# Kernel tuning notes

Measured on AMD Instinct MI355X. Metric: run time of the kernel, lower is better.

## Reference

```python
import jax, jax.numpy as jnp
import numpy as np

ITERS = 3
LAMB = 0.05
EPS = 1e-6


def _l2norm(x):
    return x / jnp.clip(jnp.linalg.norm(x, axis=-1, keepdims=True), 1e-8)


def setup_inputs() -> dict:
    key = jax.random.key(0)
    k1, k2, k3, k4 = jax.random.split(key, 4)
    bi, bt, R, W, D = 128, 128, 36, 50, 256
    imgs = jax.random.normal(k1, (bi, R, D), dtype=jnp.float32)
    caps = jax.random.normal(k2, (bt, W, D), dtype=jnp.float32)
    # valid lengths in [1, max]; pin element 0 to max so int(lens.max()) == static dim
    img_lens = jax.random.randint(k3, (bi,), 1, R + 1).at[0].set(R)
    cap_lens = jax.random.randint(k4, (bt,), 1, W + 1).at[0].set(W)
    return {"imgs": imgs, "caps": caps, "img_lens": img_lens, "cap_lens": cap_lens}


def _forward(imgs, caps, img_lens, cap_lens):
    bi, R, D = imgs.shape
    bt, W, _ = caps.shape
    # fine-grained cosine similarities: [bi, bt, R, W]
    fg_sims = jnp.einsum("ird,jwd->ijrw", _l2norm(imgs), _l2norm(caps))
    # mask[i,j,r,w] = (r < img_lens[i]) & (w < cap_lens[j])
    rmask = jnp.arange(R) < img_lens[:, None]          # [bi, R]
    wmask = jnp.arange(W) < cap_lens[:, None]          # [bt, W]
    mask = rmask[:, None, :, None] & wmask[None, :, None, :]  # [bi, bt, R, W]
    maskf = mask.astype(fg_sims.dtype)

    # _ave_init: uniform marginals over valid rows / cols
    r = (mask.sum(axis=-1) != 0).astype(fg_sims.dtype)  # [bi, bt, R]
    r = r / r.sum(axis=-1, keepdims=True)
    c = (mask.sum(axis=-2) != 0).astype(fg_sims.dtype)  # [bi, bt, W]
    c = c / c.sum(axis=-1, keepdims=True)

    # Sinkhorn-Knopp on cost (1 - sims); masked entries get cost=INF -> P=0
    P = jnp.where(mask, jnp.exp(-(1.0 - fg_sims) / LAMB), 0.0)
    P = P / (P.sum(axis=(-2, -1), keepdims=True) + EPS)

    def body(P, _):
        u = P.sum(axis=-1) + EPS          # [bi, bt, R]
        P = P * (r / u)[..., :, None]
        v = P.sum(axis=-2) + EPS          # [bi, bt, W]
        P = P * (c / v)[..., None, :]
        return P, None

    P, _ = jax.lax.scan(body, P, None, length=ITERS)
    sims = (fg_sims * P * maskf).sum(axis=(-2, -1))     # [bi, bt]
    return sims


def reference(imgs, caps, img_lens, cap_lens):
    return _forward(imgs, caps, img_lens, cap_lens)
```

## Files before the change

kernel.cpp:

```cpp
#include <hip/hip_runtime.h>
#include <math.h>

#define BI 128
#define BT 128
#define RR 36
#define WW 50
#define DD 256
#define EPSF 1e-6f
#define EXP2_C1 28.85390081777927f
#define EXP2_C0 (-28.85390081777927f)

#define A_TILES 3
#define B_TILES 4
#define KSTEPS 8
#define A_SLOTS (BI * A_TILES * KSTEPS * 64)
#define B_SLOTS (BT * B_TILES * KSTEPS * 64)

#define CV_AT (BI * A_TILES)
#define CV_BT (BT * B_TILES)

typedef short     v8ss __attribute__((ext_vector_type(8)));
typedef _Float16  v8hf __attribute__((ext_vector_type(8)));
typedef float     v4f  __attribute__((ext_vector_type(4)));

template <typename V>
__device__ __forceinline__ auto mfma_impl(V a, V b, v4f c, int)
    -> decltype(__builtin_amdgcn_mfma_f32_16x16x32_f16(a, b, c, 0, 0, 0)) {
    return __builtin_amdgcn_mfma_f32_16x16x32_f16(a, b, c, 0, 0, 0);
}
template <typename V>
__device__ __forceinline__ v4f mfma_impl(V a, V b, v4f c, long) {
    v8ss a2 = __builtin_bit_cast(v8ss, a);
    v8ss b2 = __builtin_bit_cast(v8ss, b);
    return __builtin_amdgcn_mfma_f32_16x16x32_f16(a2, b2, c, 0, 0, 0);
}
__device__ __forceinline__ v4f mfma_f16(v8hf a, v8hf b, v4f c) {
    return mfma_impl(a, b, c, 0);
}

__device__ __forceinline__ float fast_rcp(float x) {
    return __builtin_amdgcn_rcpf(x);
}
__device__ __forceinline__ float fast_exp2(float x) {
    return __builtin_amdgcn_exp2f(x);
}

template <int N>
__device__ __forceinline__ float dpp_ror_add(float x) {
    int xi = __builtin_bit_cast(int, x);
    int yi = __builtin_amdgcn_update_dpp(xi, xi, 0x120 | N, 0xF, 0xF, false);
    return x + __builtin_bit_cast(float, yi);
}
__device__ __forceinline__ float dpp_sum16(float x) {
    x = dpp_ror_add<1>(x);
    x = dpp_ror_add<2>(x);
    x = dpp_ror_add<4>(x);
    x = dpp_ror_add<8>(x);
    return x;
}

__global__ __launch_bounds__(256) void convert_kernel(
    const float* __restrict__ imgs, const float* __restrict__ caps,
    v8ss* __restrict__ Ah_g, v8ss* __restrict__ Bh_g)
{
    __shared__ float raw[16][260];
    __shared__ float invn[16];

    const int t = threadIdx.x;
    const int b = blockIdx.x;
    const bool isA = b < CV_AT;
    int grp, tile, nrows;
    const float* src;
    if (isA) {
        grp = b / A_TILES; tile = b - grp * A_TILES;
        src = imgs + (size_t)grp * RR * DD;
        nrows = RR;
    } else {
        int bb = b - CV_AT;
        grp = bb / B_TILES; tile = bb - grp * B_TILES;
        src = caps + (size_t)grp * WW * DD;
        nrows = WW;
    }
    const size_t tbase = isA ? (size_t)b * (KSTEPS * 64)
                             : (size_t)(b - CV_AT) * (KSTEPS * 64);
    const int r0 = tile << 4;

    for (int f = t; f < 1024; f += 256) {
        const int row = f >> 6, c4 = f & 63;
        float4 v = make_float4(0.f, 0.f, 0.f, 0.f);
        const int r = r0 + row;
        if (r < nrows) v = *(const float4*)(src + (size_t)r * DD + c4 * 4);
        *(float4*)&raw[row][c4 * 4] = v;
    }
    __syncthreads();

    {
        const int row = t >> 4, seg = t & 15;
        float ss = 0.f;
#pragma unroll
        for (int k = 0; k < 16; ++k) {
            float x = raw[row][k * 16 + seg];
            ss += x * x;
        }
        ss = dpp_sum16(ss);
        if (seg == 0) invn[row] = 1.0f / fmaxf(sqrtf(ss), 1e-8f);
    }
    __syncthreads();

    for (int u = t; u < KSTEPS * 64; u += 256) {
        const int ks = u >> 6, sl = u & 63;
        const int rr = sl & 15, kq = sl >> 4;
        const float inv = invn[rr];
        const float* p = &raw[rr][ks * 32 + kq * 8];
        float4 f0 = *(const float4*)p;
        float4 f1 = *(const float4*)(p + 4);
        float xs[8] = {f0.x, f0.y, f0.z, f0.w, f1.x, f1.y, f1.z, f1.w};
        v8hf h;
#pragma unroll
        for (int e = 0; e < 8; ++e) h[e] = (_Float16)(xs[e] * inv);
        if (isA) Ah_g[tbase + (size_t)ks * 64 + sl] = __builtin_bit_cast(v8ss, h);
        else     Bh_g[tbase + (size_t)ks * 64 + sl] = __builtin_bit_cast(v8ss, h);
    }
}

__global__ __launch_bounds__(64, 4) void pair_kernel(
    const v8ss* __restrict__ Ah_g, const v8ss* __restrict__ Bh_g,
    const int* __restrict__ img_lens, const int* __restrict__ cap_lens,
    float* __restrict__ out)
{
    const int lane = threadIdx.x;
    const int x    = blockIdx.x & 7;
    const int g    = blockIdx.x >> 3;
    const int i    = g >> 4;
    const int j    = (x << 4) + (g & 15);

    const int nr = img_lens[i];
    const int nc = cap_lens[j];
    const int Ma = (nr + 15) >> 4;
    const int Na = (nc + 15) >> 4;

    const v8ss* Ah_b = Ah_g + (size_t)i * (A_TILES * KSTEPS * 64) + lane;
    const v8ss* Bh_b = Bh_g + (size_t)j * (B_TILES * KSTEPS * 64) + lane;

    v4f acc[3][4];
#pragma unroll
    for (int m = 0; m < 3; ++m)
#pragma unroll
        for (int n = 0; n < 4; ++n) acc[m][n] = (v4f){0.f, 0.f, 0.f, 0.f};

    v8hf ah[2][3], bh[2][4];
    auto load_stage = [&](int ks, int buf) {
#pragma unroll
        for (int m = 0; m < 3; ++m) if (m < Ma)
            ah[buf][m] = __builtin_bit_cast(v8hf, Ah_b[(m * KSTEPS + ks) * 64]);
#pragma unroll
        for (int n = 0; n < 4; ++n) if (n < Na)
            bh[buf][n] = __builtin_bit_cast(v8hf, Bh_b[(n * KSTEPS + ks) * 64]);
    };

    load_stage(0, 0);
#pragma unroll
    for (int ks = 0; ks < KSTEPS; ++ks) {
        const int cur = ks & 1;
        if (ks + 1 < KSTEPS) load_stage(ks + 1, cur ^ 1);
#pragma unroll
        for (int n = 0; n < 4; ++n) if (n < Na)
#pragma unroll
            for (int m = 0; m < 3; ++m) if (m < Ma)
                acc[m][n] = mfma_f16(ah[cur][m], bh[cur][n], acc[m][n]);
    }

    const int cl = lane & 15;
    const int rq = (lane >> 4) << 2;
    const float inv_nr = 1.0f / (float)nr;
    const float inv_nc = 1.0f / (float)nc;

    float P0[3][4][4];
    float tot = 0.f;
#pragma unroll
    for (int m = 0; m < 3; ++m) if (m < Ma)
#pragma unroll
        for (int n = 0; n < 4; ++n) if (n < Na)
#pragma unroll
            for (int q = 0; q < 4; ++q) {
                const int row = (m << 4) + rq + q;
                const int col = (n << 4) + cl;
                float pv = 0.f;
                if (row < nr && col < nc)
                    pv = fast_exp2(fmaf(acc[m][n][q], EXP2_C1, EXP2_C0));
                P0[m][n][q] = pv;
                tot += pv;
            }
    tot = dpp_sum16(tot);
    tot += __shfl_xor(tot, 16, 64);
    tot += __shfl_xor(tot, 32, 64);
    const float gsc = fast_rcp(tot + EPSF);

    float u[3][4], v[4];
#pragma unroll
    for (int m = 0; m < 3; ++m)
#pragma unroll
        for (int q = 0; q < 4; ++q) u[m][q] = gsc;
#pragma unroll
    for (int n = 0; n < 4; ++n) v[n] = 1.0f;

#pragma unroll
    for (int it = 0; it < 3; ++it) {
#pragma unroll
        for (int m = 0; m < 3; ++m) if (m < Ma)
#pragma unroll
            for (int q = 0; q < 4; ++q) {
                float d = 0.f;
#pragma unroll
                for (int n = 0; n < 4; ++n) if (n < Na)
                    d = fmaf(P0[m][n][q], v[n], d);
                d = dpp_sum16(d);
                const float t = fmaf(u[m][q], d, EPSF);
                u[m][q] *= inv_nr * fast_rcp(t);
            }
#pragma unroll
        for (int n = 0; n < 4; ++n) if (n < Na) {
            float e = 0.f;
#pragma unroll
            for (int m = 0; m < 3; ++m) if (m < Ma)
#pragma unroll
                for (int q = 0; q < 4; ++q)
                    e = fmaf(P0[m][n][q], u[m][q], e);
            e += __shfl_xor(e, 16, 64);
            e += __shfl_xor(e, 32, 64);
            const float t = fmaf(v[n], e, EPSF);
            v[n] *= inv_nc * fast_rcp(t);
        }
    }

    float osum = 0.f;
#pragma unroll
    for (int m = 0; m < 3; ++m) if (m < Ma)
#pragma unroll
        for (int n = 0; n < 4; ++n) if (n < Na)
#pragma unroll
            for (int q = 0; q < 4; ++q)
                osum = fmaf(acc[m][n][q], P0[m][n][q] * u[m][q] * v[n], osum);
    osum = dpp_sum16(osum);
    osum += __shfl_xor(osum, 16, 64);
    osum += __shfl_xor(osum, 32, 64);
    if (lane == 0) out[i * BT + j] = osum;
}

extern "C" void kernel_launch(void* const* d_in, const int* in_sizes, int n_in,
                              void* d_out, int out_size, void* d_ws, size_t ws_size,
                              hipStream_t stream) {
    const float* imgs     = (const float*)d_in[0];
    const float* caps     = (const float*)d_in[1];
    const int*   img_lens = (const int*)d_in[2];
    const int*   cap_lens = (const int*)d_in[3];
    float* out = (float*)d_out;

    v8ss* Ah_g = (v8ss*)d_ws;
    v8ss* Bh_g = Ah_g + A_SLOTS;

    hipLaunchKernelGGL(convert_kernel, dim3(CV_AT + CV_BT), dim3(256), 0, stream,
                       imgs, caps, Ah_g, Bh_g);
    hipLaunchKernelGGL(pair_kernel, dim3(BI * BT), dim3(64), 0, stream,
                       Ah_g, Bh_g, img_lens, cap_lens, out);
}
```

Measured before the change: 109.8 us.

## Share caption tile in LDS across four image waves and rewrite convert per-row

```diff
diff --git a/kernel.cpp b/kernel.cpp
--- a/kernel.cpp
+++ b/kernel.cpp
@@ -16,11 +16,12 @@
 #define A_SLOTS (BI * A_TILES * KSTEPS * 64)
 #define B_SLOTS (BT * B_TILES * KSTEPS * 64)
 
-#define CV_AT (BI * A_TILES)
-#define CV_BT (BT * B_TILES)
+#define AVROWS (BI * 48)
+#define NVROWS (AVROWS + BT * 64)
 
 typedef short     v8ss __attribute__((ext_vector_type(8)));
 typedef _Float16  v8hf __attribute__((ext_vector_type(8)));
+typedef _Float16  v4hf __attribute__((ext_vector_type(4)));
 typedef float     v4f  __attribute__((ext_vector_type(4)));
 
 template <typename V>
@@ -63,84 +64,78 @@
     const float* __restrict__ imgs, const float* __restrict__ caps,
     v8ss* __restrict__ Ah_g, v8ss* __restrict__ Bh_g)
 {
-    __shared__ float raw[16][260];
-    __shared__ float invn[16];
-
-    const int t = threadIdx.x;
-    const int b = blockIdx.x;
-    const bool isA = b < CV_AT;
-    int grp, tile, nrows;
+    const int gid  = blockIdx.x * 256 + threadIdx.x;
+    const int wv   = gid >> 6;
+    const int lane = gid & 63;
+
+    const bool isA = wv < AVROWS;
+    int grp, r, nrows;
     const float* src;
+    v8ss* dst;
+    size_t tbase;
     if (isA) {
-        grp = b / A_TILES; tile = b - grp * A_TILES;
-        src = imgs + (size_t)grp * RR * DD;
-        nrows = RR;
+        grp = wv / 48; r = wv - grp * 48;
+        src = imgs + ((size_t)grp * RR + r) * DD;
+        nrows = RR; dst = Ah_g;
+        tbase = (size_t)(grp * A_TILES + (r >> 4)) * KSTEPS;
     } else {
-        int bb = b - CV_AT;
-        grp = bb / B_TILES; tile = bb - grp * B_TILES;
-        src = caps + (size_t)grp * WW * DD;
-        nrows = WW;
-    }
-    const size_t tbase = isA ? (size_t)b * (KSTEPS * 64)
-                             : (size_t)(b - CV_AT) * (KSTEPS * 64);
-    const int r0 = tile << 4;
-
-    for (int f = t; f < 1024; f += 256) {
-        const int row = f >> 6, c4 = f & 63;
-        float4 v = make_float4(0.f, 0.f, 0.f, 0.f);
-        const int r = r0 + row;
-        if (r < nrows) v = *(const float4*)(src + (size_t)r * DD + c4 * 4);
-        *(float4*)&raw[row][c4 * 4] = v;
-    }
-    __syncthreads();
-
-    {
-        const int row = t >> 4, seg = t & 15;
-        float ss = 0.f;
-#pragma unroll
-        for (int k = 0; k < 16; ++k) {
-            float x = raw[row][k * 16 + seg];
-            ss += x * x;
-        }
-        ss = dpp_sum16(ss);
-        if (seg == 0) invn[row] = 1.0f / fmaxf(sqrtf(ss), 1e-8f);
-    }
-    __syncthreads();
-
-    for (int u = t; u < KSTEPS * 64; u += 256) {
-        const int ks = u >> 6, sl = u & 63;
-        const int rr = sl & 15, kq = sl >> 4;
-        const float inv = invn[rr];
-        const float* p = &raw[rr][ks * 32 + kq * 8];
-        float4 f0 = *(const float4*)p;
-        float4 f1 = *(const float4*)(p + 4);
-        float xs[8] = {f0.x, f0.y, f0.z, f0.w, f1.x, f1.y, f1.z, f1.w};
-        v8hf h;
-#pragma unroll
-        for (int e = 0; e < 8; ++e) h[e] = (_Float16)(xs[e] * inv);
-        if (isA) Ah_g[tbase + (size_t)ks * 64 + sl] = __builtin_bit_cast(v8ss, h);
-        else     Bh_g[tbase + (size_t)ks * 64 + sl] = __builtin_bit_cast(v8ss, h);
-    }
-}
-
-__global__ __launch_bounds__(64, 4) void pair_kernel(
+        const int v = wv - AVROWS;
+        grp = v >> 6; r = v & 63;
+        src = caps + ((size_t)grp * WW + r) * DD;
+        nrows = WW; dst = Bh_g;
+        tbase = (size_t)(grp * B_TILES + (r >> 4)) * KSTEPS;
+    }
+    const bool valid = r < nrows;
+
+    float4 x = make_float4(0.f, 0.f, 0.f, 0.f);
+    if (valid) x = ((const float4*)src)[lane];
+    float ss = x.x * x.x + x.y * x.y + x.z * x.z + x.w * x.w;
+#pragma unroll
+    for (int off = 1; off < 64; off <<= 1) ss += __shfl_xor(ss, off, 64);
+    const float inv = valid ? 1.0f / fmaxf(sqrtf(ss), 1e-8f) : 0.f;
+
+    v4hf h;
+    h[0] = (_Float16)(x.x * inv);
+    h[1] = (_Float16)(x.y * inv);
+    h[2] = (_Float16)(x.z * inv);
+    h[3] = (_Float16)(x.w * inv);
+
+    const int rr = r & 15;
+    const int ks = lane >> 3;
+    const int kq = (lane >> 1) & 3;
+    const size_t slot = (tbase + ks) * 64 + rr + (kq << 4);
+    ((uint2*)dst)[slot * 2 + (lane & 1)] = __builtin_bit_cast(uint2, h);
+}
+
+__global__ __launch_bounds__(256, 4) void pair_kernel(
     const v8ss* __restrict__ Ah_g, const v8ss* __restrict__ Bh_g,
     const int* __restrict__ img_lens, const int* __restrict__ cap_lens,
     float* __restrict__ out)
 {
-    const int lane = threadIdx.x;
+    __shared__ v8ss Bs[B_TILES * KSTEPS * 64];
+
+    const int tid  = threadIdx.x;
+    const int lane = tid & 63;
+    const int w    = tid >> 6;
     const int x    = blockIdx.x & 7;
-    const int g    = blockIdx.x >> 3;
-    const int i    = g >> 4;
-    const int j    = (x << 4) + (g & 15);
-
+    const int jg   = (blockIdx.x >> 3) & 15;
+    const int ig   = blockIdx.x >> 7;
+    const int j    = (x << 4) + jg;
+    const int i    = ig + (w << 5);
+
+    const int nc = cap_lens[j];
+    const int Na = (nc + 15) >> 4;
     const int nr = img_lens[i];
-    const int nc = cap_lens[j];
     const int Ma = (nr + 15) >> 4;
-    const int Na = (nc + 15) >> 4;
+
+    {
+        const v8ss* Bj = Bh_g + (size_t)j * (B_TILES * KSTEPS * 64);
+        const int nslot = Na * (KSTEPS * 64);
+        for (int s = tid; s < nslot; s += 256) Bs[s] = Bj[s];
+    }
+    __syncthreads();
 
     const v8ss* Ah_b = Ah_g + (size_t)i * (A_TILES * KSTEPS * 64) + lane;
-    const v8ss* Bh_b = Bh_g + (size_t)j * (B_TILES * KSTEPS * 64) + lane;
 
     v4f acc[3][4];
 #pragma unroll
@@ -149,20 +144,26 @@
         for (int n = 0; n < 4; ++n) acc[m][n] = (v4f){0.f, 0.f, 0.f, 0.f};
 
     v8hf ah[2][3], bh[2][4];
-    auto load_stage = [&](int ks, int buf) {
+    auto load_A = [&](int ks, int buf) {
 #pragma unroll
         for (int m = 0; m < 3; ++m) if (m < Ma)
             ah[buf][m] = __builtin_bit_cast(v8hf, Ah_b[(m * KSTEPS + ks) * 64]);
-#pragma unroll
-        for (int n = 0; n < 4; ++n) if (n < Na)
-            bh[buf][n] = __builtin_bit_cast(v8hf, Bh_b[(n * KSTEPS + ks) * 64]);
     };
-
-    load_stage(0, 0);
+    auto read_B = [&](int ks, int buf) {
+#pragma unroll
+        for (int n = 0; n < 4; ++n) if (n < Na)
+            bh[buf][n] = __builtin_bit_cast(v8hf, Bs[(n * KSTEPS + ks) * 64 + lane]);
+    };
+
+    load_A(0, 0);
+    read_B(0, 0);
 #pragma unroll
     for (int ks = 0; ks < KSTEPS; ++ks) {
         const int cur = ks & 1;
-        if (ks + 1 < KSTEPS) load_stage(ks + 1, cur ^ 1);
+        if (ks + 1 < KSTEPS) {
+            load_A(ks + 1, cur ^ 1);
+            read_B(ks + 1, cur ^ 1);
+        }
 #pragma unroll
         for (int n = 0; n < 4; ++n) if (n < Na)
 #pragma unroll
@@ -233,14 +234,18 @@
         }
     }
 
-    float osum = 0.f;
+    float os0 = 0.f, os1 = 0.f;
 #pragma unroll
     for (int m = 0; m < 3; ++m) if (m < Ma)
 #pragma unroll
         for (int n = 0; n < 4; ++n) if (n < Na)
 #pragma unroll
-            for (int q = 0; q < 4; ++q)
-                osum = fmaf(acc[m][n][q], P0[m][n][q] * u[m][q] * v[n], osum);
+            for (int q = 0; q < 4; ++q) {
+                const float t = P0[m][n][q] * u[m][q] * v[n];
+                if (q & 1) os1 = fmaf(acc[m][n][q], t, os1);
+                else       os0 = fmaf(acc[m][n][q], t, os0);
+            }
+    float osum = os0 + os1;
     osum = dpp_sum16(osum);
     osum += __shfl_xor(osum, 16, 64);
     osum += __shfl_xor(osum, 32, 64);
@@ -259,8 +264,8 @@
     v8ss* Ah_g = (v8ss*)d_ws;
     v8ss* Bh_g = Ah_g + A_SLOTS;
 
-    hipLaunchKernelGGL(convert_kernel, dim3(CV_AT + CV_BT), dim3(256), 0, stream,
+    hipLaunchKernelGGL(convert_kernel, dim3(NVROWS * 64 / 256), dim3(256), 0, stream,
                        imgs, caps, Ah_g, Bh_g);
-    hipLaunchKernelGGL(pair_kernel, dim3(BI * BT), dim3(64), 0, stream,
+    hipLaunchKernelGGL(pair_kernel, dim3(BI * BT / 4), dim3(256), 0, stream,
                        Ah_g, Bh_g, img_lens, cap_lens, out);
 }
```

Measured after the change: 114.6 us. +4.3%, slower.
